# Optimization experiments

Hardware: AMD Instinct MI355X
Metric: run time of the kernel (lower is better)

## Reference

```python
import jax, jax.numpy as jnp
import numpy as np

SD, MD, HM, HR, N_STEPS = 64, 64, 128, 128, 10
N_VARS, DEG = 2048, 8


def _build_graph():
    rng = np.random.default_rng(0)
    n = N_VARS
    us = np.repeat(np.arange(n), 4)
    ks = np.tile(np.arange(1, 5), n)
    vs = (us + ks) % n
    factors = np.stack([np.minimum(us, vs), np.maximum(us, vs)], 1)  # [F,2], u<v
    F = factors.shape[0]
    J = np.zeros((n, n), np.float32)
    vals = rng.normal(size=F).astype(np.float32)
    J[factors[:, 0], factors[:, 1]] = vals
    J[factors[:, 1], factors[:, 0]] = vals
    b = rng.normal(size=n).astype(np.float32)
    var_node = factors.reshape(-1)          # variable of each message node
    fac_node = np.repeat(np.arange(F), 2)   # factor of each message node
    M = var_node.shape[0]
    order = np.argsort(var_node, kind='stable').reshape(n, DEG)
    jj = np.broadcast_to(order[:, :, None], (n, DEG, DEG))
    ii = np.broadcast_to(order[:, None, :], (n, DEG, DEG))
    mask = fac_node[jj] != fac_node[ii]     # same variable, different factor
    f2v_row = jj[mask].astype(np.int64)
    f2v_col = ii[mask].astype(np.int64)
    fu = fac_node[f2v_row]; fv = fac_node[f2v_col]
    feat5 = np.stack([b[var_node[f2v_col]],
                      J[factors[fu, 0], factors[fu, 1]], J[factors[fu, 1], factors[fu, 0]],
                      J[factors[fv, 0], factors[fv, 1]], J[factors[fv, 1], factors[fv, 0]]], 1).astype(np.float32)
    v2f_row = np.arange(M, dtype=np.int64)
    v2f_col = v2f_row ^ 1                   # same factor, other variable
    f = fac_node[v2f_row]
    feat4 = np.stack([b[var_node[v2f_row]], b[var_node[v2f_col]],
                      J[factors[f, 0], factors[f, 1]], J[factors[f, 1], factors[f, 0]]], 1).astype(np.float32)
    return f2v_row, f2v_col, feat5, v2f_row, v2f_col, feat4, var_node.astype(np.int64), M


def setup_inputs():
    f2v_row, f2v_col, feat5, v2f_row, v2f_col, feat4, readout_col, M = _build_graph()
    rng = np.random.default_rng(1)
    def lin(o, i):
        return rng.normal(0, 0.1, size=(o, i)).astype(np.float32), np.zeros(o, np.float32)
    def gru_p():
        s = 1.0 / np.sqrt(SD)
        return tuple(rng.uniform(-s, s, sh).astype(np.float32)
                     for sh in ((3 * SD, MD), (3 * SD, SD), (3 * SD,), (3 * SD,)))
    d = {}
    d['attn_W'], d['attn_b'] = lin(1, 2 * SD)
    d['v2f_W1'], d['v2f_b1'] = lin(HM, 2 * SD + 5)
    d['v2f_W2'], d['v2f_b2'] = lin(HM, HM)
    d['v2f_W3'], d['v2f_b3'] = lin(MD, HM)
    d['f2v_W1'], d['f2v_b1'] = lin(HM, 2 * SD + 4)
    d['f2v_W2'], d['f2v_b2'] = lin(HM, HM)
    d['f2v_W3'], d['f2v_b3'] = lin(MD, HM)
    d['ro_W1'], d['ro_b1'] = lin(HR, SD)
    d['ro_W2'], d['ro_b2'] = lin(HR, HR)
    d['ro_W3'], d['ro_b3'] = lin(2, HR)
    d['gv_Wi'], d['gv_Wh'], d['gv_bi'], d['gv_bh'] = gru_p()
    d['gf_Wi'], d['gf_Wh'], d['gf_bi'], d['gf_bh'] = gru_p()
    d = {k: jnp.asarray(v) for k, v in d.items()}
    d.update(feat5=jnp.asarray(feat5), feat4=jnp.asarray(feat4),
             f2v_row=jnp.asarray(f2v_row), f2v_col=jnp.asarray(f2v_col),
             v2f_row=jnp.asarray(v2f_row), v2f_col=jnp.asarray(v2f_col),
             readout_col=jnp.asarray(readout_col), n_vars=N_VARS, n_msg=int(M))
    return d


def _mlp3(x, W1, b1, W2, b2, W3, b3):
    h = jax.nn.relu(x @ W1.T + b1)
    h = jax.nn.relu(h @ W2.T + b2)
    return h @ W3.T + b3


def _gru(x, h, Wi, Wh, bi, bh):
    gi = x @ Wi.T + bi
    gh = h @ Wh.T + bh
    ir, iz, in_ = jnp.split(gi, 3, -1)
    hr, hz, hn = jnp.split(gh, 3, -1)
    r = jax.nn.sigmoid(ir + hr)
    z = jax.nn.sigmoid(iz + hz)
    n = jnp.tanh(in_ + r * hn)
    return (1.0 - z) * n + z * h


def reference(attn_W, attn_b, v2f_W1, v2f_b1, v2f_W2, v2f_b2, v2f_W3, v2f_b3,
              f2v_W1, f2v_b1, f2v_W2, f2v_b2, f2v_W3, f2v_b3,
              ro_W1, ro_b1, ro_W2, ro_b2, ro_W3, ro_b3,
              gv_Wi, gv_Wh, gv_bi, gv_bh, gf_Wi, gf_Wh, gf_bi, gf_bh,
              feat5, feat4, f2v_row, f2v_col, v2f_row, v2f_col, readout_col, n_vars, n_msg):
    v2f_h = jnp.zeros((n_msg, SD), feat5.dtype)
    f2v_h = jnp.zeros((n_msg, SD), feat5.dtype)

    def attn(hi, hj):
        e = jax.nn.leaky_relu(jnp.concatenate([hi, hj], -1) @ attn_W.T + attn_b)
        return jax.nn.softmax(e, axis=0)  # global softmax over all edges, shape [E,1]

    for _ in range(N_STEPS):
        hi = f2v_h[f2v_row]; hj = v2f_h[f2v_col]
        msg = _mlp3(jnp.concatenate([hi, hj, feat5], -1),
                    v2f_W1, v2f_b1, v2f_W2, v2f_b2, v2f_W3, v2f_b3) * attn(hi, hj)
        v2f_h = _gru(jax.ops.segment_sum(msg, f2v_col, num_segments=n_msg),
                     v2f_h, gv_Wi, gv_Wh, gv_bi, gv_bh)
        hi = v2f_h[v2f_row]; hj = f2v_h[v2f_col]
        msg = _mlp3(jnp.concatenate([hi, hj, feat4], -1),
                    f2v_W1, f2v_b1, f2v_W2, f2v_b2, f2v_W3, f2v_b3) * attn(hi, hj)
        f2v_h = _gru(jax.ops.segment_sum(msg, v2f_col, num_segments=n_msg),
                     f2v_h, gf_Wi, gf_Wh, gf_bi, gf_bh)

    node = jax.ops.segment_sum(f2v_h, readout_col, num_segments=n_vars)
    return jax.nn.softmax(_mlp3(node, ro_W1, ro_b1, ro_W2, ro_b2, ro_W3, ro_b3), axis=1)
```

## Files before the change

### kernel.cpp

```cpp
#include <hip/hip_runtime.h>
#include <cstdint>
#include <cstddef>

#define E1C 114688
#define MMC 16384
#define NVC 2048
#define NSTEPS 10

typedef __bf16 bf16x8 __attribute__((ext_vector_type(8)));
typedef float  f32x4  __attribute__((ext_vector_type(4)));

__device__ __forceinline__ float sigm(float x) { return 1.0f / (1.0f + expf(-x)); }
__device__ __forceinline__ bf16x8 ld8(const __bf16* p) {
  return *reinterpret_cast<const bf16x8*>(p);
}

#define NJOBS 13
struct PrepJobs {
  const float* src[NJOBS];
  __bf16* dst0;
  int kin[NJOBS];
  int nin[NJOBS];
  int ntile[NJOBS];
  int base[NJOBS];
  int total;
};

__global__ __launch_bounds__(256) void k_prep_all(PrepJobs J) {
  int gid = blockIdx.x * 256 + threadIdx.x;
  if (gid >= J.total) return;
  int jb = 0;
  #pragma unroll
  for (int x = 1; x < NJOBS; ++x) if (gid >= J.base[x]) jb = x;
  int d = gid - J.base[jb];
  int group = d >> 9, rr = d & 511, ln = rr >> 3, j = rr & 7;
  int q = ln >> 4, m16 = ln & 15;
  int NT = J.ntile[jb];
  int kc = group / NT, nt = group - kc * NT;
  int n = nt * 16 + m16, k = kc * 32 + q * 8 + j;
  int kin = J.kin[jb];
  float v = (k < kin && n < J.nin[jb]) ? J.src[jb][(size_t)n * kin + k] : 0.f;
  J.dst0[gid] = (__bf16)v;
}

template<int FDIM, int EPB>
__global__ __launch_bounds__(256, 3) void k_mlp(
    const float* __restrict__ hA, const float* __restrict__ hB,
    const int* __restrict__ rowIdx, const int* __restrict__ colIdx,
    const float* __restrict__ feat,
    const __bf16* __restrict__ W1f, const float* __restrict__ b1,
    const __bf16* __restrict__ W2f, const float* __restrict__ b2,
    const __bf16* __restrict__ W3f, const float* __restrict__ b3,
    const float* __restrict__ attnW, const float* __restrict__ attnB,
    float* __restrict__ msgOut, float* __restrict__ eOut,
    float* __restrict__ Zpart)
{
  constexpr int RPW = EPB / 4;
  constexpr int MTILES = EPB / 16;
  constexpr int LPE = 64 / RPW;
  __shared__ __align__(16) __bf16 Xs[EPB][168];
  __shared__ float zp[4];
  const int t = threadIdx.x, lane = t & 63, w = t >> 6;
  const int r0 = w * RPW;
  const int e0 = blockIdx.x * EPB;

  {
    const int half = lane >> 5, l2 = lane & 31;
    const float* hbase = half ? hB : hA;
    const int* ibase = half ? colIdx : rowIdx;
    #pragma unroll
    for (int i = 0; i < RPW; ++i) {
      int e = r0 + i;
      int idx = ibase[e0 + e];
      float2 v = *reinterpret_cast<const float2*>(hbase + (size_t)idx * 64 + l2 * 2);
      union { __bf16 b[2]; unsigned u; } cv;
      cv.b[0] = (__bf16)v.x; cv.b[1] = (__bf16)v.y;
      *reinterpret_cast<unsigned*>(&Xs[e][half * 64 + l2 * 2]) = cv.u;
    }
    #pragma unroll
    for (int it = 0; it < RPW / 2; ++it) {
      int e = r0 + it * 2 + (lane >> 5);
      int f = lane & 31;
      float fv = (f < FDIM) ? feat[(size_t)(e0 + e) * FDIM + f] : 0.f;
      Xs[e][128 + f] = (__bf16)fv;
    }
  }

  {
    constexpr int ND = 128 / LPE;
    int eL = r0 + lane / LPE, part = lane & (LPE - 1);
    float s = 0.f;
    #pragma unroll
    for (int jj = 0; jj < ND / 8; ++jj) {
      bf16x8 xv = ld8(&Xs[eL][part * ND + jj * 8]);
      #pragma unroll
      for (int j = 0; j < 8; ++j) s += attnW[part * ND + jj * 8 + j] * (float)xv[j];
    }
    s += __shfl_xor(s, 1);
    if (LPE == 4) s += __shfl_xor(s, 2);
    float ex = 0.f;
    if (part == 0) {
      float le = s + attnB[0];
      le = le > 0.f ? le : 0.01f * le;
      eOut[e0 + eL] = le;
      ex = expf(le);
    }
    #pragma unroll
    for (int off = 1; off < 64; off <<= 1) ex += __shfl_xor(ex, off);
    if (lane == 0) zp[w] = ex;
  }
  __syncthreads();
  if (t == 0) Zpart[blockIdx.x] = zp[0] + zp[1] + zp[2] + zp[3];

  const int m16 = lane & 15, q = lane >> 4;

  {
    bf16x8 B0[5], B1[5];
    #pragma unroll
    for (int kc = 0; kc < 5; ++kc) {
      B0[kc] = ld8(W1f + (size_t)(kc * 8 + w * 2 + 0) * 512 + lane * 8);
      B1[kc] = ld8(W1f + (size_t)(kc * 8 + w * 2 + 1) * 512 + lane * 8);
    }
    f32x4 a0[MTILES], a1[MTILES];
    float bv0 = b1[(w * 2) * 16 + m16], bv1 = b1[(w * 2 + 1) * 16 + m16];
    #pragma unroll
    for (int mt = 0; mt < MTILES; ++mt) {
      a0[mt] = (f32x4){bv0, bv0, bv0, bv0};
      a1[mt] = (f32x4){bv1, bv1, bv1, bv1};
      #pragma unroll
      for (int kc = 0; kc < 5; ++kc) {
        bf16x8 av = ld8(&Xs[mt * 16 + m16][kc * 32 + q * 8]);
        a0[mt] = __builtin_amdgcn_mfma_f32_16x16x32_bf16(av, B0[kc], a0[mt], 0, 0, 0);
        a1[mt] = __builtin_amdgcn_mfma_f32_16x16x32_bf16(av, B1[kc], a1[mt], 0, 0, 0);
      }
    }
    __syncthreads();
    #pragma unroll
    for (int mt = 0; mt < MTILES; ++mt)
      #pragma unroll
      for (int r2 = 0; r2 < 4; ++r2) {
        float v0 = a0[mt][r2]; v0 = v0 > 0.f ? v0 : 0.f;
        float v1 = a1[mt][r2]; v1 = v1 > 0.f ? v1 : 0.f;
        Xs[mt * 16 + q * 4 + r2][(w * 2) * 16 + m16]     = (__bf16)v0;
        Xs[mt * 16 + q * 4 + r2][(w * 2 + 1) * 16 + m16] = (__bf16)v1;
      }
    __syncthreads();
  }

  {
    bf16x8 B0[4], B1[4];
    #pragma unroll
    for (int kc = 0; kc < 4; ++kc) {
      B0[kc] = ld8(W2f + (size_t)(kc * 8 + w * 2 + 0) * 512 + lane * 8);
      B1[kc] = ld8(W2f + (size_t)(kc * 8 + w * 2 + 1) * 512 + lane * 8);
    }
    f32x4 a0[MTILES], a1[MTILES];
    float bv0 = b2[(w * 2) * 16 + m16], bv1 = b2[(w * 2 + 1) * 16 + m16];
    #pragma unroll
    for (int mt = 0; mt < MTILES; ++mt) {
      a0[mt] = (f32x4){bv0, bv0, bv0, bv0};
      a1[mt] = (f32x4){bv1, bv1, bv1, bv1};
      #pragma unroll
      for (int kc = 0; kc < 4; ++kc) {
        bf16x8 av = ld8(&Xs[mt * 16 + m16][kc * 32 + q * 8]);
        a0[mt] = __builtin_amdgcn_mfma_f32_16x16x32_bf16(av, B0[kc], a0[mt], 0, 0, 0);
        a1[mt] = __builtin_amdgcn_mfma_f32_16x16x32_bf16(av, B1[kc], a1[mt], 0, 0, 0);
      }
    }
    __syncthreads();
    #pragma unroll
    for (int mt = 0; mt < MTILES; ++mt)
      #pragma unroll
      for (int r2 = 0; r2 < 4; ++r2) {
        float v0 = a0[mt][r2]; v0 = v0 > 0.f ? v0 : 0.f;
        float v1 = a1[mt][r2]; v1 = v1 > 0.f ? v1 : 0.f;
        Xs[mt * 16 + q * 4 + r2][(w * 2) * 16 + m16]     = (__bf16)v0;
        Xs[mt * 16 + q * 4 + r2][(w * 2 + 1) * 16 + m16] = (__bf16)v1;
      }
    __syncthreads();
  }

  {
    bf16x8 B3[4];
    #pragma unroll
    for (int kc = 0; kc < 4; ++kc)
      B3[kc] = ld8(W3f + (size_t)(kc * 4 + w) * 512 + lane * 8);
    float bv = b3[w * 16 + m16];
    #pragma unroll
    for (int mt = 0; mt < MTILES; ++mt) {
      f32x4 acc = (f32x4){bv, bv, bv, bv};
      #pragma unroll
      for (int kc = 0; kc < 4; ++kc) {
        bf16x8 av = ld8(&Xs[mt * 16 + m16][kc * 32 + q * 8]);
        acc = __builtin_amdgcn_mfma_f32_16x16x32_bf16(av, B3[kc], acc, 0, 0, 0);
      }
      #pragma unroll
      for (int r2 = 0; r2 < 4; ++r2)
        msgOut[(size_t)(e0 + mt * 16 + q * 4 + r2) * 64 + w * 16 + m16] = acc[r2];
    }
  }
}

__global__ __launch_bounds__(256) void k_agg_gru(
    const float* __restrict__ msg, const float* __restrict__ eatt,
    const float* __restrict__ Zp, int zn,
    const int* __restrict__ colIdx, float* __restrict__ hbuf,
    const __bf16* __restrict__ WiF, const __bf16* __restrict__ WhF,
    const float* __restrict__ bi, const float* __restrict__ bh, int mode)
{
  __shared__ __align__(16) __bf16 xsf[4096];
  __shared__ __align__(16) __bf16 hsf[4096];
  __shared__ float hs32[64][68];
  __shared__ float wexp[64][8];
  __shared__ int mloc[64];
  __shared__ float zred[4];
  const int t = threadIdx.x, lane = t & 63, w = t >> 6;
  const int vb0 = blockIdx.x * 64;

  {
    float zs = 0.f;
    for (int i = t; i < zn; i += 256) zs += Zp[i];
    #pragma unroll
    for (int off = 32; off; off >>= 1) zs += __shfl_down(zs, off);
    if (lane == 0) zred[w] = zs;
  }
  __syncthreads();
  const float invZ = 1.0f / (zred[0] + zred[1] + zred[2] + zred[3]);

  if (mode == 0) {
    for (int idx = t; idx < 448; idx += 256) {
      int i = idx / 7, a1 = idx - i * 7;
      int vb = vb0 + i, v = vb >> 3, b = vb & 7;
      int a = a1 + (a1 >= b ? 1 : 0);
      int ed = v * 56 + a * 7 + b - (b > a ? 1 : 0);
      wexp[i][a1] = expf(eatt[ed]) * invZ;
    }
    if (t < 64) {
      int vb = vb0 + t, v = vb >> 3, b = vb & 7;
      mloc[t] = colIdx[v * 56 + (b == 0 ? 7 : b - 1)];
    }
  } else {
    if (t < 64) mloc[t] = vb0 + t;
  }
  __syncthreads();

  {
    const int i = t >> 2, cb = t & 3;
    float sum[16];
    #pragma unroll
    for (int c = 0; c < 16; ++c) sum[c] = 0.f;
    if (mode == 0) {
      int vb = vb0 + i, v = vb >> 3, b = vb & 7;
      #pragma unroll
      for (int a1 = 0; a1 < 7; ++a1) {
        int a = a1 + (a1 >= b ? 1 : 0);
        int ed = v * 56 + a * 7 + b - (b > a ? 1 : 0);
        float wgt = wexp[i][a1];
        const float4* mp = (const float4*)(msg + (size_t)ed * 64 + cb * 16);
        float4 m0 = mp[0], m1 = mp[1], m2 = mp[2], m3 = mp[3];
        sum[0]  += wgt * m0.x; sum[1]  += wgt * m0.y; sum[2]  += wgt * m0.z; sum[3]  += wgt * m0.w;
        sum[4]  += wgt * m1.x; sum[5]  += wgt * m1.y; sum[6]  += wgt * m1.z; sum[7]  += wgt * m1.w;
        sum[8]  += wgt * m2.x; sum[9]  += wgt * m2.y; sum[10] += wgt * m2.z; sum[11] += wgt * m2.w;
        sum[12] += wgt * m3.x; sum[13] += wgt * m3.y; sum[14] += wgt * m3.z; sum[15] += wgt * m3.w;
      }
    } else {
      int src = colIdx[vb0 + i];
      float wgt = expf(eatt[src]) * invZ;
      const float4* mp = (const float4*)(msg + (size_t)src * 64 + cb * 16);
      float4 m0 = mp[0], m1 = mp[1], m2 = mp[2], m3 = mp[3];
      sum[0]  = wgt * m0.x; sum[1]  = wgt * m0.y; sum[2]  = wgt * m0.z; sum[3]  = wgt * m0.w;
      sum[4]  = wgt * m1.x; sum[5]  = wgt * m1.y; sum[6]  = wgt * m1.z; sum[7]  = wgt * m1.w;
      sum[8]  = wgt * m2.x; sum[9]  = wgt * m2.y; sum[10] = wgt * m2.z; sum[11] = wgt * m2.w;
      sum[12] = wgt * m3.x; sum[13] = wgt * m3.y; sum[14] = wgt * m3.z; sum[15] = wgt * m3.w;
    }
    #pragma unroll
    for (int half = 0; half < 2; ++half) {
      __bf16 v8[8];
      #pragma unroll
      for (int j = 0; j < 8; ++j) v8[j] = (__bf16)sum[half * 8 + j];
      int addr = (i >> 4) * 1024 + (cb >> 1) * 512 + ((cb & 1) * 2 + half) * 128 + (i & 15) * 8;
      *(uint4*)(xsf + addr) = *(const uint4*)v8;
    }
    const float4* hp = (const float4*)(hbuf + (size_t)mloc[i] * 64 + cb * 16);
    float4 h4[4] = {hp[0], hp[1], hp[2], hp[3]};
    *(float4*)(&hs32[i][cb * 16 + 0])  = h4[0];
    *(float4*)(&hs32[i][cb * 16 + 4])  = h4[1];
    *(float4*)(&hs32[i][cb * 16 + 8])  = h4[2];
    *(float4*)(&hs32[i][cb * 16 + 12]) = h4[3];
    const float* hf = (const float*)h4;
    #pragma unroll
    for (int half = 0; half < 2; ++half) {
      __bf16 v8[8];
      #pragma unroll
      for (int j = 0; j < 8; ++j) v8[j] = (__bf16)hf[half * 8 + j];
      int addr = (i >> 4) * 1024 + (cb >> 1) * 512 + ((cb & 1) * 2 + half) * 128 + (i & 15) * 8;
      *(uint4*)(hsf + addr) = *(const uint4*)v8;
    }
  }
  __syncthreads();

  const int m16 = lane & 15, q = lane >> 4;
  f32x4 gi[12], gh[12];
  #pragma unroll
  for (int nt = 0; nt < 12; ++nt) { gi[nt] = (f32x4){0,0,0,0}; gh[nt] = (f32x4){0,0,0,0}; }
  #pragma unroll
  for (int kc = 0; kc < 2; ++kc) {
    bf16x8 ax = ld8(xsf + w * 1024 + kc * 512 + lane * 8);
    bf16x8 ah = ld8(hsf + w * 1024 + kc * 512 + lane * 8);
    #pragma unroll
    for (int nt = 0; nt < 12; ++nt) {
      bf16x8 bx = ld8(WiF + (size_t)(kc * 12 + nt) * 512 + lane * 8);
      gi[nt] = __builtin_amdgcn_mfma_f32_16x16x32_bf16(ax, bx, gi[nt], 0, 0, 0);
      bf16x8 bh8 = ld8(WhF + (size_t)(kc * 12 + nt) * 512 + lane * 8);
      gh[nt] = __builtin_amdgcn_mfma_f32_16x16x32_bf16(ah, bh8, gh[nt], 0, 0, 0);
    }
  }

  #pragma unroll
  for (int nt = 0; nt < 4; ++nt) {
    int o = nt * 16 + m16;
    float bir = bi[o]       + bh[o];
    float biz = bi[64 + o]  + bh[64 + o];
    float bin = bi[128 + o], bhn = bh[128 + o];
    #pragma unroll
    for (int r = 0; r < 4; ++r) {
      int nl = w * 16 + q * 4 + r;
      float rg = sigm(gi[nt][r]     + gh[nt][r]     + bir);
      float zg = sigm(gi[nt + 4][r] + gh[nt + 4][r] + biz);
      float ng = tanhf(gi[nt + 8][r] + bin + rg * (gh[nt + 8][r] + bhn));
      float ho = hs32[nl][o];
      hbuf[(size_t)mloc[nl] * 64 + o] = (1.f - zg) * ng + zg * ho;
    }
  }
}

__global__ __launch_bounds__(256) void k_readout(
    const float* __restrict__ f2v_h, const int* __restrict__ f2v_col,
    const __bf16* __restrict__ W1f, const float* __restrict__ b1,
    const __bf16* __restrict__ W2f, const float* __restrict__ b2,
    const __bf16* __restrict__ W3f, const float* __restrict__ b3,
    float* __restrict__ out)
{
  __shared__ __align__(16) __bf16 Xs[64][136];
  const int t = threadIdx.x, lane = t & 63, w = t >> 6;
  const int r0 = w * 16;
  const int v0 = blockIdx.x * 64;

  #pragma unroll
  for (int i = 0; i < 16; ++i) {
    int v = v0 + r0 + i;
    float s = 0.f;
    #pragma unroll
    for (int b = 0; b < 8; ++b) {
      int m = f2v_col[v * 56 + (b == 0 ? 7 : (b - 1))];
      s += f2v_h[(size_t)m * 64 + lane];
    }
    Xs[r0 + i][lane] = (__bf16)s;
  }

  const int m16 = lane & 15, q = lane >> 4;

  {
    f32x4 acc[8];
    #pragma unroll
    for (int nt = 0; nt < 8; ++nt) {
      float bv = b1[nt * 16 + m16];
      acc[nt] = (f32x4){bv, bv, bv, bv};
    }
    #pragma unroll
    for (int kc = 0; kc < 2; ++kc) {
      bf16x8 av = ld8(&Xs[r0 + m16][kc * 32 + q * 8]);
      #pragma unroll
      for (int nt = 0; nt < 8; ++nt) {
        bf16x8 bv = ld8(W1f + (size_t)(kc * 8 + nt) * 512 + lane * 8);
        acc[nt] = __builtin_amdgcn_mfma_f32_16x16x32_bf16(av, bv, acc[nt], 0, 0, 0);
      }
    }
    #pragma unroll
    for (int nt = 0; nt < 8; ++nt)
      #pragma unroll
      for (int r2 = 0; r2 < 4; ++r2) {
        float v = acc[nt][r2]; v = v > 0.f ? v : 0.f;
        Xs[r0 + q * 4 + r2][nt * 16 + m16] = (__bf16)v;
      }
  }

  {
    f32x4 acc[8];
    #pragma unroll
    for (int nt = 0; nt < 8; ++nt) {
      float bv = b2[nt * 16 + m16];
      acc[nt] = (f32x4){bv, bv, bv, bv};
    }
    #pragma unroll
    for (int kc = 0; kc < 4; ++kc) {
      bf16x8 av = ld8(&Xs[r0 + m16][kc * 32 + q * 8]);
      #pragma unroll
      for (int nt = 0; nt < 8; ++nt) {
        bf16x8 bv = ld8(W2f + (size_t)(kc * 8 + nt) * 512 + lane * 8);
        acc[nt] = __builtin_amdgcn_mfma_f32_16x16x32_bf16(av, bv, acc[nt], 0, 0, 0);
      }
    }
    #pragma unroll
    for (int nt = 0; nt < 8; ++nt)
      #pragma unroll
      for (int r2 = 0; r2 < 4; ++r2) {
        float v = acc[nt][r2]; v = v > 0.f ? v : 0.f;
        Xs[r0 + q * 4 + r2][nt * 16 + m16] = (__bf16)v;
      }
  }

  {
    f32x4 acc = (f32x4){0, 0, 0, 0};
    if (m16 < 2) { float bv = b3[m16]; acc = (f32x4){bv, bv, bv, bv}; }
    #pragma unroll
    for (int kc = 0; kc < 4; ++kc) {
      bf16x8 av = ld8(&Xs[r0 + m16][kc * 32 + q * 8]);
      bf16x8 bv = ld8(W3f + (size_t)kc * 512 + lane * 8);
      acc = __builtin_amdgcn_mfma_f32_16x16x32_bf16(av, bv, acc, 0, 0, 0);
    }
    #pragma unroll
    for (int r = 0; r < 4; ++r) {
      float other = __shfl_xor(acc[r], 1);
      if (m16 == 0) {
        float l0 = acc[r], l1 = other;
        float mx = fmaxf(l0, l1);
        float p0 = expf(l0 - mx), p1 = expf(l1 - mx);
        float inv = 1.0f / (p0 + p1);
        int v = v0 + r0 + q * 4 + r;
        *reinterpret_cast<float2*>(out + (size_t)v * 2) = make_float2(p0 * inv, p1 * inv);
      }
    }
  }
}

extern "C" void kernel_launch(void* const* d_in, const int* in_sizes, int n_in,
                              void* d_out, int out_size, void* d_ws, size_t ws_size,
                              hipStream_t stream) {
  const float* attn_W = (const float*)d_in[0];
  const float* attn_b = (const float*)d_in[1];
  const float* v2f_W1 = (const float*)d_in[2];
  const float* v2f_b1 = (const float*)d_in[3];
  const float* v2f_W2 = (const float*)d_in[4];
  const float* v2f_b2 = (const float*)d_in[5];
  const float* v2f_W3 = (const float*)d_in[6];
  const float* v2f_b3 = (const float*)d_in[7];
  const float* f2v_W1 = (const float*)d_in[8];
  const float* f2v_b1 = (const float*)d_in[9];
  const float* f2v_W2 = (const float*)d_in[10];
  const float* f2v_b2 = (const float*)d_in[11];
  const float* f2v_W3 = (const float*)d_in[12];
  const float* f2v_b3 = (const float*)d_in[13];
  const float* ro_W1  = (const float*)d_in[14];
  const float* ro_b1  = (const float*)d_in[15];
  const float* ro_W2  = (const float*)d_in[16];
  const float* ro_b2  = (const float*)d_in[17];
  const float* ro_W3  = (const float*)d_in[18];
  const float* ro_b3  = (const float*)d_in[19];
  const float* gv_Wi  = (const float*)d_in[20];
  const float* gv_Wh  = (const float*)d_in[21];
  const float* gv_bi  = (const float*)d_in[22];
  const float* gv_bh  = (const float*)d_in[23];
  const float* gf_Wi  = (const float*)d_in[24];
  const float* gf_Wh  = (const float*)d_in[25];
  const float* gf_bi  = (const float*)d_in[26];
  const float* gf_bh  = (const float*)d_in[27];
  const float* feat5  = (const float*)d_in[28];
  const float* feat4  = (const float*)d_in[29];
  const int* f2v_row  = (const int*)d_in[30];
  const int* f2v_col  = (const int*)d_in[31];
  const int* v2f_row  = (const int*)d_in[32];
  const int* v2f_col  = (const int*)d_in[33];

  float* ws = (float*)d_ws;
  float* msg    = ws;
  float* eatt   = msg + (size_t)E1C * 64;
  float* h_v2f  = eatt + E1C;
  float* h_f2v  = h_v2f + (size_t)MMC * 64;
  float* Zp     = h_f2v + (size_t)MMC * 64;
  __bf16* wbuf  = (__bf16*)(((uintptr_t)(Zp + 20 * 1024) + 15) & ~(uintptr_t)15);
  __bf16* w1v = wbuf;
  __bf16* w2v = w1v + 20480;
  __bf16* w3v = w2v + 16384;
  __bf16* w1f = w3v + 8192;
  __bf16* w2f = w1f + 20480;
  __bf16* w3f = w2f + 16384;
  __bf16* wiv = w3f + 8192;
  __bf16* whv = wiv + 12288;
  __bf16* wif = whv + 12288;
  __bf16* whf = wif + 12288;
  __bf16* wr1 = whf + 12288;
  __bf16* wr2 = wr1 + 8192;
  __bf16* wr3 = wr2 + 16384;

  hipMemsetAsync(h_v2f, 0, (size_t)2 * MMC * 64 * sizeof(float), stream);

  {
    PrepJobs J;
    const float* srcs[NJOBS] = {v2f_W1, v2f_W2, v2f_W3, f2v_W1, f2v_W2, f2v_W3,
                                gv_Wi, gv_Wh, gf_Wi, gf_Wh, ro_W1, ro_W2, ro_W3};
    int kin[NJOBS]  = {133, 128, 128, 132, 128, 128, 64, 64, 64, 64, 64, 128, 128};
    int nin[NJOBS]  = {128, 128, 64, 128, 128, 64, 192, 192, 192, 192, 128, 128, 2};
    int nt[NJOBS]   = {8, 8, 4, 8, 8, 4, 12, 12, 12, 12, 8, 8, 1};
    int size[NJOBS] = {20480, 16384, 8192, 20480, 16384, 8192,
                       12288, 12288, 12288, 12288, 8192, 16384, 2048};
    int cum = 0;
    for (int i = 0; i < NJOBS; ++i) {
      J.src[i] = srcs[i]; J.kin[i] = kin[i]; J.nin[i] = nin[i]; J.ntile[i] = nt[i];
      J.base[i] = cum; cum += size[i];
    }
    J.dst0 = wbuf; J.total = cum;
    k_prep_all<<<(cum + 255) / 256, 256, 0, stream>>>(J);
  }

  const int ZN1 = E1C / 128;
  const int ZN2 = MMC / 64;

  for (int s = 0; s < NSTEPS; ++s) {
    float* z1 = Zp + (size_t)(s * 2) * 1024;
    float* z2 = Zp + (size_t)(s * 2 + 1) * 1024;
    k_mlp<5, 128><<<E1C / 128, 256, 0, stream>>>(
        h_f2v, h_v2f, f2v_row, f2v_col, feat5,
        w1v, v2f_b1, w2v, v2f_b2, w3v, v2f_b3,
        attn_W, attn_b, msg, eatt, z1);
    k_agg_gru<<<MMC / 64, 256, 0, stream>>>(
        msg, eatt, z1, ZN1, f2v_col, h_v2f,
        wiv, whv, gv_bi, gv_bh, 0);
    k_mlp<4, 64><<<MMC / 64, 256, 0, stream>>>(
        h_v2f, h_f2v, v2f_row, v2f_col, feat4,
        w1f, f2v_b1, w2f, f2v_b2, w3f, f2v_b3,
        attn_W, attn_b, msg, eatt, z2);
    k_agg_gru<<<MMC / 64, 256, 0, stream>>>(
        msg, eatt, z2, ZN2, v2f_col, h_f2v,
        wif, whf, gf_bi, gf_bh, 1);
  }
  k_readout<<<NVC / 64, 256, 0, stream>>>(h_f2v, f2v_col,
                                          wr1, ro_b1, wr2, ro_b2, wr3, ro_b3,
                                          (float*)d_out);
}
```

Before: 798.7 us.

## Fuse attention-weighted segment sum into MLP kernel, drop message round trip

The edge MLP kernel now multiplies each message by its unnormalized attention exponent and performs the per-node segment sum in shared memory. The f2v block size changes to 112 edges so whole variables (56 edges each) fall within one block, and the v2f pairing swap is done in place. The GRU kernel then reads a dense pre-aggregated input scaled by 1/Z instead of gathering the full per-edge message and attention arrays. This removes the large E×64 message write and re-read between kernels. In exchange it adds extra shared-memory passes and syncs in the MLP kernel, and a non-power-of-two tile with partly idle lanes in the attention dot product.

```diff
diff --git a/kernel.cpp b/kernel.cpp
--- a/kernel.cpp
+++ b/kernel.cpp
@@ -43,7 +43,7 @@
   J.dst0[gid] = (__bf16)v;
 }
 
-template<int FDIM, int EPB>
+template<int FDIM, int EPB, int MODE>
 __global__ __launch_bounds__(256, 3) void k_mlp(
     const float* __restrict__ hA, const float* __restrict__ hB,
     const int* __restrict__ rowIdx, const int* __restrict__ colIdx,
@@ -52,14 +52,17 @@
     const __bf16* __restrict__ W2f, const float* __restrict__ b2,
     const __bf16* __restrict__ W3f, const float* __restrict__ b3,
     const float* __restrict__ attnW, const float* __restrict__ attnB,
-    float* __restrict__ msgOut, float* __restrict__ eOut,
-    float* __restrict__ Zpart)
+    float* __restrict__ xout, float* __restrict__ Zpart)
 {
   constexpr int RPW = EPB / 4;
   constexpr int MTILES = EPB / 16;
-  constexpr int LPE = 64 / RPW;
+  constexpr int LPE = (EPB == 112) ? 2 : 4;
+  constexpr int ACT = RPW * LPE;
+  constexpr int ND = 128 / LPE;
   __shared__ __align__(16) __bf16 Xs[EPB][168];
+  __shared__ float wexp[EPB];
   __shared__ float zp[4];
+  __shared__ int mloc[16];
   const int t = threadIdx.x, lane = t & 63, w = t >> 6;
   const int r0 = w * RPW;
   const int e0 = blockIdx.x * EPB;
@@ -86,24 +89,31 @@
     }
   }
 
-  {
-    constexpr int ND = 128 / LPE;
-    int eL = r0 + lane / LPE, part = lane & (LPE - 1);
+  if (MODE == 0 && t < 16) {
+    int v = blockIdx.x * 2 + (t >> 3), b = t & 7;
+    mloc[t] = colIdx[v * 56 + (b == 0 ? 7 : b - 1)];
+  }
+
+  {
+    int eL = r0 + lane / LPE, part = lane % LPE;
+    bool act = (lane < ACT);
     float s = 0.f;
-    #pragma unroll
-    for (int jj = 0; jj < ND / 8; ++jj) {
-      bf16x8 xv = ld8(&Xs[eL][part * ND + jj * 8]);
-      #pragma unroll
-      for (int j = 0; j < 8; ++j) s += attnW[part * ND + jj * 8 + j] * (float)xv[j];
+    if (act) {
+      #pragma unroll
+      for (int jj = 0; jj < ND / 8; ++jj) {
+        bf16x8 xv = ld8(&Xs[eL][part * ND + jj * 8]);
+        #pragma unroll
+        for (int j = 0; j < 8; ++j) s += attnW[part * ND + jj * 8 + j] * (float)xv[j];
+      }
     }
     s += __shfl_xor(s, 1);
     if (LPE == 4) s += __shfl_xor(s, 2);
     float ex = 0.f;
-    if (part == 0) {
+    if (act && part == 0) {
       float le = s + attnB[0];
       le = le > 0.f ? le : 0.01f * le;
-      eOut[e0 + eL] = le;
       ex = expf(le);
+      wexp[eL] = ex;
     }
     #pragma unroll
     for (int off = 1; off < 64; off <<= 1) ex += __shfl_xor(ex, off);
@@ -180,6 +190,7 @@
     __syncthreads();
   }
 
+  f32x4 a3[MTILES];
   {
     bf16x8 B3[4];
     #pragma unroll
@@ -188,34 +199,61 @@
     float bv = b3[w * 16 + m16];
     #pragma unroll
     for (int mt = 0; mt < MTILES; ++mt) {
-      f32x4 acc = (f32x4){bv, bv, bv, bv};
+      a3[mt] = (f32x4){bv, bv, bv, bv};
       #pragma unroll
       for (int kc = 0; kc < 4; ++kc) {
         bf16x8 av = ld8(&Xs[mt * 16 + m16][kc * 32 + q * 8]);
-        acc = __builtin_amdgcn_mfma_f32_16x16x32_bf16(av, B3[kc], acc, 0, 0, 0);
-      }
-      #pragma unroll
-      for (int r2 = 0; r2 < 4; ++r2)
-        msgOut[(size_t)(e0 + mt * 16 + q * 4 + r2) * 64 + w * 16 + m16] = acc[r2];
+        a3[mt] = __builtin_amdgcn_mfma_f32_16x16x32_bf16(av, B3[kc], a3[mt], 0, 0, 0);
+      }
+    }
+  }
+  __syncthreads();
+
+  float* Ms = reinterpret_cast<float*>(&Xs[0][0]);
+  #pragma unroll
+  for (int mt = 0; mt < MTILES; ++mt)
+    #pragma unroll
+    for (int r2 = 0; r2 < 4; ++r2) {
+      int e = mt * 16 + q * 4 + r2;
+      Ms[e * 68 + w * 16 + m16] = wexp[e] * a3[mt][r2];
+    }
+  __syncthreads();
+
+  if (MODE == 0) {
+    int node = t >> 4, cg = t & 15;
+    int vloc = node >> 3, b = node & 7;
+    float4 s4 = make_float4(0.f, 0.f, 0.f, 0.f);
+    #pragma unroll
+    for (int a1 = 0; a1 < 7; ++a1) {
+      int a = a1 + (a1 >= b ? 1 : 0);
+      int e = vloc * 56 + a * 7 + b - (b > a ? 1 : 0);
+      float4 mv = *reinterpret_cast<const float4*>(Ms + e * 68 + cg * 4);
+      s4.x += mv.x; s4.y += mv.y; s4.z += mv.z; s4.w += mv.w;
+    }
+    *reinterpret_cast<float4*>(xout + (size_t)mloc[node] * 64 + cg * 4) = s4;
+  } else {
+    #pragma unroll
+    for (int it = 0; it < 4; ++it) {
+      int idx = t + it * 256;
+      int ml = idx >> 4, cg = idx & 15;
+      float4 v = *reinterpret_cast<const float4*>(Ms + (ml ^ 1) * 68 + cg * 4);
+      *reinterpret_cast<float4*>(xout + (size_t)(e0 + ml) * 64 + cg * 4) = v;
     }
   }
 }
 
-__global__ __launch_bounds__(256) void k_agg_gru(
-    const float* __restrict__ msg, const float* __restrict__ eatt,
-    const float* __restrict__ Zp, int zn,
-    const int* __restrict__ colIdx, float* __restrict__ hbuf,
+__global__ __launch_bounds__(256) void k_gru(
+    const float* __restrict__ xt, const float* __restrict__ Zp, int zn,
+    float* __restrict__ hbuf,
     const __bf16* __restrict__ WiF, const __bf16* __restrict__ WhF,
-    const float* __restrict__ bi, const float* __restrict__ bh, int mode)
+    const float* __restrict__ bi, const float* __restrict__ bh)
 {
   __shared__ __align__(16) __bf16 xsf[4096];
   __shared__ __align__(16) __bf16 hsf[4096];
   __shared__ float hs32[64][68];
-  __shared__ float wexp[64][8];
-  __shared__ int mloc[64];
   __shared__ float zred[4];
   const int t = threadIdx.x, lane = t & 63, w = t >> 6;
-  const int vb0 = blockIdx.x * 64;
+  const int n0 = blockIdx.x * 64;
 
   {
     float zs = 0.f;
@@ -227,61 +265,24 @@
   __syncthreads();
   const float invZ = 1.0f / (zred[0] + zred[1] + zred[2] + zred[3]);
 
-  if (mode == 0) {
-    for (int idx = t; idx < 448; idx += 256) {
-      int i = idx / 7, a1 = idx - i * 7;
-      int vb = vb0 + i, v = vb >> 3, b = vb & 7;
-      int a = a1 + (a1 >= b ? 1 : 0);
-      int ed = v * 56 + a * 7 + b - (b > a ? 1 : 0);
-      wexp[i][a1] = expf(eatt[ed]) * invZ;
-    }
-    if (t < 64) {
-      int vb = vb0 + t, v = vb >> 3, b = vb & 7;
-      mloc[t] = colIdx[v * 56 + (b == 0 ? 7 : b - 1)];
-    }
-  } else {
-    if (t < 64) mloc[t] = vb0 + t;
-  }
-  __syncthreads();
-
   {
     const int i = t >> 2, cb = t & 3;
-    float sum[16];
-    #pragma unroll
-    for (int c = 0; c < 16; ++c) sum[c] = 0.f;
-    if (mode == 0) {
-      int vb = vb0 + i, v = vb >> 3, b = vb & 7;
-      #pragma unroll
-      for (int a1 = 0; a1 < 7; ++a1) {
-        int a = a1 + (a1 >= b ? 1 : 0);
-        int ed = v * 56 + a * 7 + b - (b > a ? 1 : 0);
-        float wgt = wexp[i][a1];
-        const float4* mp = (const float4*)(msg + (size_t)ed * 64 + cb * 16);
-        float4 m0 = mp[0], m1 = mp[1], m2 = mp[2], m3 = mp[3];
-        sum[0]  += wgt * m0.x; sum[1]  += wgt * m0.y; sum[2]  += wgt * m0.z; sum[3]  += wgt * m0.w;
-        sum[4]  += wgt * m1.x; sum[5]  += wgt * m1.y; sum[6]  += wgt * m1.z; sum[7]  += wgt * m1.w;
-        sum[8]  += wgt * m2.x; sum[9]  += wgt * m2.y; sum[10] += wgt * m2.z; sum[11] += wgt * m2.w;
-        sum[12] += wgt * m3.x; sum[13] += wgt * m3.y; sum[14] += wgt * m3.z; sum[15] += wgt * m3.w;
-      }
-    } else {
-      int src = colIdx[vb0 + i];
-      float wgt = expf(eatt[src]) * invZ;
-      const float4* mp = (const float4*)(msg + (size_t)src * 64 + cb * 16);
-      float4 m0 = mp[0], m1 = mp[1], m2 = mp[2], m3 = mp[3];
-      sum[0]  = wgt * m0.x; sum[1]  = wgt * m0.y; sum[2]  = wgt * m0.z; sum[3]  = wgt * m0.w;
-      sum[4]  = wgt * m1.x; sum[5]  = wgt * m1.y; sum[6]  = wgt * m1.z; sum[7]  = wgt * m1.w;
-      sum[8]  = wgt * m2.x; sum[9]  = wgt * m2.y; sum[10] = wgt * m2.z; sum[11] = wgt * m2.w;
-      sum[12] = wgt * m3.x; sum[13] = wgt * m3.y; sum[14] = wgt * m3.z; sum[15] = wgt * m3.w;
-    }
+    const float4* xp = (const float4*)(xt + (size_t)(n0 + i) * 64 + cb * 16);
+    float4 x4[4] = {xp[0], xp[1], xp[2], xp[3]};
+    #pragma unroll
+    for (int k = 0; k < 4; ++k) {
+      x4[k].x *= invZ; x4[k].y *= invZ; x4[k].z *= invZ; x4[k].w *= invZ;
+    }
+    const float* xf = (const float*)x4;
     #pragma unroll
     for (int half = 0; half < 2; ++half) {
       __bf16 v8[8];
       #pragma unroll
-      for (int j = 0; j < 8; ++j) v8[j] = (__bf16)sum[half * 8 + j];
+      for (int j = 0; j < 8; ++j) v8[j] = (__bf16)xf[half * 8 + j];
       int addr = (i >> 4) * 1024 + (cb >> 1) * 512 + ((cb & 1) * 2 + half) * 128 + (i & 15) * 8;
       *(uint4*)(xsf + addr) = *(const uint4*)v8;
     }
-    const float4* hp = (const float4*)(hbuf + (size_t)mloc[i] * 64 + cb * 16);
+    const float4* hp = (const float4*)(hbuf + (size_t)(n0 + i) * 64 + cb * 16);
     float4 h4[4] = {hp[0], hp[1], hp[2], hp[3]};
     *(float4*)(&hs32[i][cb * 16 + 0])  = h4[0];
     *(float4*)(&hs32[i][cb * 16 + 4])  = h4[1];
@@ -329,7 +330,7 @@
       float zg = sigm(gi[nt + 4][r] + gh[nt + 4][r] + biz);
       float ng = tanhf(gi[nt + 8][r] + bin + rg * (gh[nt + 8][r] + bhn));
       float ho = hs32[nl][o];
-      hbuf[(size_t)mloc[nl] * 64 + o] = (1.f - zg) * ng + zg * ho;
+      hbuf[(size_t)(n0 + nl) * 64 + o] = (1.f - zg) * ng + zg * ho;
     }
   }
 }
@@ -473,9 +474,9 @@
   const int* v2f_col  = (const int*)d_in[33];
 
   float* ws = (float*)d_ws;
-  float* msg    = ws;
-  float* eatt   = msg + (size_t)E1C * 64;
-  float* h_v2f  = eatt + E1C;
+  float* xt1    = ws;
+  float* xt2    = xt1 + (size_t)MMC * 64;
+  float* h_v2f  = xt2 + (size_t)MMC * 64;
   float* h_f2v  = h_v2f + (size_t)MMC * 64;
   float* Zp     = h_f2v + (size_t)MMC * 64;
   __bf16* wbuf  = (__bf16*)(((uintptr_t)(Zp + 20 * 1024) + 15) & ~(uintptr_t)15);
@@ -513,26 +514,24 @@
     k_prep_all<<<(cum + 255) / 256, 256, 0, stream>>>(J);
   }
 
-  const int ZN1 = E1C / 128;
+  const int ZN1 = E1C / 112;
   const int ZN2 = MMC / 64;
 
   for (int s = 0; s < NSTEPS; ++s) {
     float* z1 = Zp + (size_t)(s * 2) * 1024;
     float* z2 = Zp + (size_t)(s * 2 + 1) * 1024;
-    k_mlp<5, 128><<<E1C / 128, 256, 0, stream>>>(
+    k_mlp<5, 112, 0><<<E1C / 112, 256, 0, stream>>>(
         h_f2v, h_v2f, f2v_row, f2v_col, feat5,
         w1v, v2f_b1, w2v, v2f_b2, w3v, v2f_b3,
-        attn_W, attn_b, msg, eatt, z1);
-    k_agg_gru<<<MMC / 64, 256, 0, stream>>>(
-        msg, eatt, z1, ZN1, f2v_col, h_v2f,
-        wiv, whv, gv_bi, gv_bh, 0);
-    k_mlp<4, 64><<<MMC / 64, 256, 0, stream>>>(
+        attn_W, attn_b, xt1, z1);
+    k_gru<<<MMC / 64, 256, 0, stream>>>(xt1, z1, ZN1, h_v2f,
+                                        wiv, whv, gv_bi, gv_bh);
+    k_mlp<4, 64, 1><<<MMC / 64, 256, 0, stream>>>(
         h_v2f, h_f2v, v2f_row, v2f_col, feat4,
         w1f, f2v_b1, w2f, f2v_b2, w3f, f2v_b3,
-        attn_W, attn_b, msg, eatt, z2);
-    k_agg_gru<<<MMC / 64, 256, 0, stream>>>(
-        msg, eatt, z2, ZN2, v2f_col, h_f2v,
-        wif, whf, gf_bi, gf_bh, 1);
+        attn_W, attn_b, xt2, z2);
+    k_gru<<<MMC / 64, 256, 0, stream>>>(xt2, z2, ZN2, h_f2v,
+                                        wif, whf, gf_bi, gf_bh);
   }
   k_readout<<<NVC / 64, 256, 0, stream>>>(h_f2v, f2v_col,
                                           wr1, ro_b1, wr2, ro_b2, wr3, ro_b3,
```

Result: faster. 682.6 us (-14.5%).
